# Performance work log

Hardware: AMD Instinct MI355X
Metric: run time of the kernel (lower is better)

## Reference

```python
import jax, jax.numpy as jnp
import numpy as np
from jax import lax

PLENS = [2, 3, 4, 5, 6, 7]
NPAT = 50  # patterns per length
V, WD, T, H, C = 100000, 300, 2048, 100, 2
D = sum(p * 2 * NPAT for p in PLENS)  # 2700 diag rows actually used


def setup_inputs() -> dict:
    key = jax.random.key(0)
    ks = jax.random.split(key, 20)
    inp = {}
    inp['doc'] = jax.random.randint(ks[0], (T,), 0, V)
    inp['embeddings'] = jax.random.normal(ks[1], (V, WD), jnp.float32)
    diags = jax.random.normal(ks[2], (D, WD), jnp.float32)
    diags = diags / jnp.linalg.norm(diags, axis=1, keepdims=True)  # normalize() in __init__
    inp['diags'] = diags
    inp['bias'] = jax.random.normal(ks[3], (D,), jnp.float32)
    for i, p in enumerate(PLENS):
        inp[f'eps{p}'] = jax.random.normal(ks[4 + i], (NPAT, p - 1), jnp.float32)
    inp['epsilon_scale'] = 0.5 * jnp.ones((1,), jnp.float32)
    inp['self_loop_scale'] = 0.5 * jnp.ones((1,), jnp.float32)
    tot = NPAT * len(PLENS)  # 300
    inp['w1'] = jax.random.normal(ks[10], (tot, H), jnp.float32) * 0.05
    inp['b1'] = jax.random.normal(ks[11], (H,), jnp.float32) * 0.05
    inp['w2'] = jax.random.normal(ks[12], (H, C), jnp.float32) * 0.05
    inp['b2'] = jax.random.normal(ks[13], (C,), jnp.float32) * 0.05
    return inp


def _run_group(tm, eps, sls, plen):
    # tm: [T, NPAT, 2, plen]; eps: [NPAT, plen-1]; sls: [1] (self-loop scale)
    # sum-times semiring: zero=0, one=1, plus=add, times=mul
    one_col = jnp.ones((NPAT, 1), tm.dtype)
    zero_col = jnp.zeros((NPAT, 1), tm.dtype)
    h0 = jnp.concatenate([one_col, jnp.zeros((NPAT, plen - 1), tm.dtype)], axis=1)

    def step(carry, tm_t):
        h, sc = carry
        # epsilon transitions
        h = h + jnp.concatenate([zero_col, h[:, :-1] * eps], axis=1)
        # main (word) transitions with restart padding (semiring one)
        res = jnp.concatenate([one_col, h[:, :-1] * tm_t[:, 1, :-1]], axis=1)
        # scaled self-loops
        res = res + sls * (h * tm_t[:, 0, :])
        return (res, sc + res[:, -1]), None

    (_, sc), _ = lax.scan(step, (h0, jnp.zeros((NPAT,), tm.dtype)), tm)
    return sc  # [NPAT]


def reference(doc, embeddings, diags, bias, eps2, eps3, eps4, eps5, eps6, eps7,
              epsilon_scale, self_loop_scale, w1, b1, w2, b2):
    # all per-token transition values at once: [T, D]
    tm_full = jax.nn.sigmoid(embeddings[doc] @ diags.T + bias)
    sls = jax.nn.sigmoid(self_loop_scale)
    eps_sc = jax.nn.sigmoid(epsilon_scale)
    eps_list = [eps2, eps3, eps4, eps5, eps6, eps7]
    scores = []
    start = 0
    for p, eps_raw in zip(PLENS, eps_list):
        end = start + p * 2 * NPAT
        tm = tm_full[:, start:end].reshape(-1, NPAT, 2, p)
        eps = eps_sc * jax.nn.sigmoid(eps_raw)
        scores.append(_run_group(tm, eps, sls, p))
        start = end
    s = jnp.concatenate(scores)[None, :]  # [1, total_num_patterns]
    h = jax.nn.relu(s @ w1 + b1)
    return h @ w2 + b2  # logits [1, num_classes]
```

## Files before the change

kernel.cpp:

```cpp
#include <hip/hip_runtime.h>
#include <math.h>

#define T_LEN 2048
#define WD 300
#define DTOT 2700
#define NPAT 50
#define H_DIM 100
#define NCLS 2
#define CCH 64
#define SCH 32
#define TOTPAT 300
#define RSTRIDE 68
#define KP 320
#define ASTR 40

typedef short bf16x8 __attribute__((ext_vector_type(8)));
typedef float f32x4 __attribute__((ext_vector_type(4)));

__device__ __forceinline__ float sigm(float x) { return 1.f / (1.f + __expf(-x)); }

__device__ __forceinline__ unsigned short f2bf(float x) {
    unsigned int u = __float_as_uint(x);
    u += 0x7fffu + ((u >> 16) & 1u);
    return (unsigned short)(u >> 16);
}
__device__ __forceinline__ float bf2f(unsigned short h) {
    return __uint_as_float(((unsigned int)h) << 16);
}

#define NA2 (T_LEN * (KP / 2))
#define NB2 (DTOT * (KP / 2))

__global__ __launch_bounds__(256) void prepack(const int* __restrict__ doc,
                                               const float* __restrict__ emb,
                                               const float* __restrict__ diags,
                                               unsigned short* __restrict__ Ah,
                                               unsigned short* __restrict__ Al,
                                               unsigned short* __restrict__ Bh,
                                               unsigned short* __restrict__ Bl) {
    int gid = blockIdx.x * 256 + threadIdx.x;
    float2 v = make_float2(0.f, 0.f);
    unsigned short* ph;
    unsigned short* pl;
    size_t off;
    if (gid < NA2) {
        int t = gid / (KP / 2);
        int kk = (gid - t * (KP / 2)) * 2;
        if (kk < WD) v = *(const float2*)(emb + (size_t)doc[t] * WD + kk);
        off = (size_t)t * KP + kk;
        ph = Ah; pl = Al;
    } else {
        int b = gid - NA2;
        if (b >= NB2) return;
        int n = b / (KP / 2);
        int kk = (b - n * (KP / 2)) * 2;
        if (kk < WD) v = *(const float2*)(diags + (size_t)n * WD + kk);
        off = (size_t)n * KP + kk;
        ph = Bh; pl = Bl;
    }
    unsigned short h0 = f2bf(v.x), h1 = f2bf(v.y);
    unsigned short l0 = f2bf(v.x - bf2f(h0)), l1 = f2bf(v.y - bf2f(h1));
    ushort2 hv; hv.x = h0; hv.y = h1;
    ushort2 lv; lv.x = l0; lv.y = l1;
    *(ushort2*)(ph + off) = hv;
    *(ushort2*)(pl + off) = lv;
}

__global__ __launch_bounds__(256) void gemm_mfma(const unsigned short* __restrict__ Ah,
                                                 const unsigned short* __restrict__ Al,
                                                 const unsigned short* __restrict__ Bh,
                                                 const unsigned short* __restrict__ Bl,
                                                 const float* __restrict__ bias,
                                                 float* __restrict__ Cm) {
    __shared__ unsigned short sA[2][128][ASTR];
    __shared__ unsigned short sB[2][64][ASTR];
    int tid = threadIdx.x;
    int lane = tid & 63, wid = tid >> 6;
    int m0 = blockIdx.y * 128, n0 = blockIdx.x * 64;
    int wm = (wid >> 1) * 64;
    int wn = (wid & 1) * 32;

    int srow = tid >> 2, sq = tid & 3;
    int nr = n0 + srow; if (nr > DTOT - 1) nr = DTOT - 1;
    const size_t a0off = (size_t)(m0 + srow) * KP + sq * 8;
    const size_t a1off = (size_t)(m0 + srow + 64) * KP + sq * 8;
    const size_t boff = (size_t)nr * KP + sq * 8;

    f32x4 acc[4][2];
#pragma unroll
    for (int mi = 0; mi < 4; ++mi)
#pragma unroll
        for (int ni = 0; ni < 2; ++ni) acc[mi][ni] = (f32x4)(0.f);

    uint4 pah0 = *(const uint4*)(Ah + a0off);
    uint4 pah1 = *(const uint4*)(Ah + a1off);
    uint4 pal0 = *(const uint4*)(Al + a0off);
    uint4 pal1 = *(const uint4*)(Al + a1off);
    uint4 pbh = *(const uint4*)(Bh + boff);
    uint4 pbl = *(const uint4*)(Bl + boff);

    for (int k0 = 0; k0 < KP; k0 += 32) {
        __syncthreads();
        *(uint4*)&sA[0][srow][sq * 8] = pah0;
        *(uint4*)&sA[0][srow + 64][sq * 8] = pah1;
        *(uint4*)&sA[1][srow][sq * 8] = pal0;
        *(uint4*)&sA[1][srow + 64][sq * 8] = pal1;
        *(uint4*)&sB[0][srow][sq * 8] = pbh;
        *(uint4*)&sB[1][srow][sq * 8] = pbl;
        __syncthreads();

        if (k0 + 32 < KP) {
            int kn = k0 + 32;
            pah0 = *(const uint4*)(Ah + a0off + kn);
            pah1 = *(const uint4*)(Ah + a1off + kn);
            pal0 = *(const uint4*)(Al + a0off + kn);
            pal1 = *(const uint4*)(Al + a1off + kn);
            pbh = *(const uint4*)(Bh + boff + kn);
            pbl = *(const uint4*)(Bl + boff + kn);
        }

        int kc = (lane >> 4) * 8;
        int mr = lane & 15;
        bf16x8 ah[4], al[4], bh[2], bl[2];
#pragma unroll
        for (int mi = 0; mi < 4; ++mi) {
            ah[mi] = *(bf16x8*)&sA[0][wm + mi * 16 + mr][kc];
            al[mi] = *(bf16x8*)&sA[1][wm + mi * 16 + mr][kc];
        }
#pragma unroll
        for (int ni = 0; ni < 2; ++ni) {
            bh[ni] = *(bf16x8*)&sB[0][wn + ni * 16 + mr][kc];
            bl[ni] = *(bf16x8*)&sB[1][wn + ni * 16 + mr][kc];
        }
#pragma unroll
        for (int mi = 0; mi < 4; ++mi)
#pragma unroll
            for (int ni = 0; ni < 2; ++ni) {
                acc[mi][ni] = __builtin_amdgcn_mfma_f32_16x16x32_bf16(ah[mi], bh[ni], acc[mi][ni], 0, 0, 0);
                acc[mi][ni] = __builtin_amdgcn_mfma_f32_16x16x32_bf16(ah[mi], bl[ni], acc[mi][ni], 0, 0, 0);
                acc[mi][ni] = __builtin_amdgcn_mfma_f32_16x16x32_bf16(al[mi], bh[ni], acc[mi][ni], 0, 0, 0);
            }
    }

    int mr = lane & 15;
    int rq = lane >> 4;
#pragma unroll
    for (int ni = 0; ni < 2; ++ni) {
        int col = n0 + wn + ni * 16 + mr;
        int cc = col < DTOT ? col : DTOT - 1;
        float bs = bias[cc];
        if (col < DTOT) {
#pragma unroll
            for (int mi = 0; mi < 4; ++mi)
#pragma unroll
                for (int r = 0; r < 4; ++r) {
                    int row = m0 + wm + mi * 16 + rq * 4 + r;
                    Cm[(size_t)row * DTOT + col] = sigm(acc[mi][ni][r] + bs);
                }
        }
    }
}

template <int P, int PBP>
__device__ void pass1_blk(int chunk, int patblk, const float* __restrict__ tm,
                          const float* __restrict__ epsr, float sls, float esc,
                          float* __restrict__ ws2, int g, float* __restrict__ sT,
                          int tid) {
    constexpr int NP1 = P + 1;
    constexpr int dstart = 100 * ((P * (P - 1)) / 2 - 1);
    constexpr int ROWF = PBP * 2 * P;
    constexpr int RB4 = ROWF / 4;
    constexpr int NF4 = SCH * RB4;

    const float* gbase = tm + (size_t)(chunk * SCH) * DTOT + dstart + patblk * ROWF;
#pragma unroll
    for (int i = 0; i < (NF4 + 63) / 64; ++i) {
        int f = i * 64 + tid;
        if (f < NF4) {
            int t = f / RB4;
            int q = f - t * RB4;
            *(float4*)&sT[t * ROWF + q * 4] = *(const float4*)(gbase + (size_t)t * DTOT + q * 4);
        }
    }
    __syncthreads();

    int patl = tid / NP1;
    int col = tid - patl * NP1;
    int pat = patblk * PBP + patl;
    if (patl < PBP && pat < NPAT) {
        float eps[P - 1];
#pragma unroll
        for (int j = 0; j < P - 1; ++j) eps[j] = esc * sigm(epsr[pat * (P - 1) + j]);

        float x[P];
#pragma unroll
        for (int i = 0; i < P; ++i) x[i] = 0.f;
        float inj = 0.f;
        if (col < P) x[col] = 1.f; else inj = 1.f;
        float qacc = 0.f;

        const float* lb = sT + patl * 2 * P;
#pragma unroll 4
        for (int t = 0; t < SCH; ++t) {
            float tv[2 * P];
            const float* row = lb + t * ROWF;
#pragma unroll
            for (int j = 0; j < P; ++j) {
                float2 u = *(const float2*)(row + 2 * j);
                tv[2 * j] = u.x;
                tv[2 * j + 1] = u.y;
            }
            float heps[P];
            heps[0] = x[0];
#pragma unroll
            for (int i = 1; i < P; ++i) heps[i] = fmaf(x[i - 1], eps[i - 1], x[i]);
            float res[P];
            res[0] = fmaf(heps[0], sls * tv[0], inj);
#pragma unroll
            for (int i = 1; i < P; ++i)
                res[i] = fmaf(heps[i - 1], tv[P + i - 1], heps[i] * (sls * tv[i]));
#pragma unroll
            for (int i = 0; i < P; ++i) x[i] = res[i];
            qacc += x[P - 1];
        }

        int gidx = g * NPAT + pat;
        float* dst = ws2 + ((size_t)(gidx * CCH + chunk)) * 64 + col * 8;
#pragma unroll
        for (int i = 0; i < P; ++i) dst[i] = x[i];
        dst[7] = qacc;
    }
}

__global__ __launch_bounds__(64) void pass1_kernel(const float* __restrict__ tm,
                                                   const float* __restrict__ e2,
                                                   const float* __restrict__ e3,
                                                   const float* __restrict__ e4,
                                                   const float* __restrict__ e5,
                                                   const float* __restrict__ e6,
                                                   const float* __restrict__ e7,
                                                   const float* __restrict__ eps_scale,
                                                   const float* __restrict__ sl_scale,
                                                   float* __restrict__ ws2) {
    __shared__ float sT[3584];
    int b = blockIdx.x;
    int chunk = b / 30;
    int r = b - chunk * 30;
    int tid = threadIdx.x;
    float sls = sigm(sl_scale[0]);
    float esc = sigm(eps_scale[0]);
    if (r < 3)       pass1_blk<2, 21>(chunk, r,      tm, e2, sls, esc, ws2, 0, sT, tid);
    else if (r < 7)  pass1_blk<3, 16>(chunk, r - 3,  tm, e3, sls, esc, ws2, 1, sT, tid);
    else if (r < 12) pass1_blk<4, 12>(chunk, r - 7,  tm, e4, sls, esc, ws2, 2, sT, tid);
    else if (r < 17) pass1_blk<5, 10>(chunk, r - 12, tm, e5, sls, esc, ws2, 3, sT, tid);
    else if (r < 23) pass1_blk<6, 9>(chunk, r - 17,  tm, e6, sls, esc, ws2, 4, sT, tid);
    else             pass1_blk<7, 8>(chunk, r - 23,  tm, e7, sls, esc, ws2, 5, sT, tid);
}

template <int P>
__device__ void fold_pattern(const float* __restrict__ ws2, float* __restrict__ R,
                             float* __restrict__ scores, int gidx, int tid) {
    constexpr int NP1 = P + 1;
    const float4* src = (const float4*)(ws2 + (size_t)gidx * CCH * 64);
#pragma unroll
    for (int j = 0; j < 4; ++j) {
        int f = j * 256 + tid;
        int rec = f >> 4;
        int q4 = f & 15;
        *(float4*)&R[rec * RSTRIDE + q4 * 4] = src[f];
    }
    int pair = tid / NP1;
    int col = tid - pair * NP1;
    for (int g = 1; g < CCH; g <<= 1) {
        __syncthreads();
        int npairs = CCH / (2 * g);
        if (pair < npairs) {
            float* Ar = &R[(pair * 2 * g) * RSTRIDE];
            const float* Br = &R[(pair * 2 * g + g) * RSTRIDE];
            if (col < P) {
                float MAj[P], mc[P];
#pragma unroll
                for (int i = 0; i < P; ++i) { MAj[i] = Ar[col * 8 + i]; mc[i] = 0.f; }
                float qc = Ar[col * 8 + 7];
#pragma unroll
                for (int k = 0; k < P; ++k) {
                    float a = MAj[k];
#pragma unroll
                    for (int i = 0; i < P; ++i) mc[i] = fmaf(Br[k * 8 + i], a, mc[i]);
                    qc = fmaf(Br[k * 8 + 7], a, qc);
                }
#pragma unroll
                for (int i = 0; i < P; ++i) Ar[col * 8 + i] = mc[i];
                Ar[col * 8 + 7] = qc;
            } else {
                float vA[P], vc[P];
#pragma unroll
                for (int i = 0; i < P; ++i) { vA[i] = Ar[P * 8 + i]; vc[i] = Br[P * 8 + i]; }
                float rc = Ar[P * 8 + 7] + Br[P * 8 + 7];
#pragma unroll
                for (int k = 0; k < P; ++k) {
                    float a = vA[k];
#pragma unroll
                    for (int i = 0; i < P; ++i) vc[i] = fmaf(Br[k * 8 + i], a, vc[i]);
                    rc = fmaf(Br[k * 8 + 7], a, rc);
                }
#pragma unroll
                for (int i = 0; i < P; ++i) Ar[P * 8 + i] = vc[i];
                Ar[P * 8 + 7] = rc;
            }
        }
    }
    __syncthreads();
    if (tid == 0) scores[gidx] = R[0 * 8 + 7] + R[P * 8 + 7];
}

__global__ __launch_bounds__(256) void pass2a_kernel(const float* __restrict__ ws2,
                                                     float* __restrict__ scores) {
    __shared__ float R[CCH * RSTRIDE];
    int gidx = blockIdx.x;
    int g = gidx / NPAT;
    int tid = threadIdx.x;
    switch (g) {
        case 0: fold_pattern<2>(ws2, R, scores, gidx, tid); break;
        case 1: fold_pattern<3>(ws2, R, scores, gidx, tid); break;
        case 2: fold_pattern<4>(ws2, R, scores, gidx, tid); break;
        case 3: fold_pattern<5>(ws2, R, scores, gidx, tid); break;
        case 4: fold_pattern<6>(ws2, R, scores, gidx, tid); break;
        case 5: fold_pattern<7>(ws2, R, scores, gidx, tid); break;
    }
}

__global__ __launch_bounds__(256) void mlp_kernel(const float* __restrict__ scores,
                                                  const float* __restrict__ w1,
                                                  const float* __restrict__ b1,
                                                  const float* __restrict__ w2,
                                                  const float* __restrict__ b2,
                                                  float* __restrict__ out) {
    __shared__ float w1_lds[TOTPAT * H_DIM];
    __shared__ float s_lds[TOTPAT];
    __shared__ float h_lds[H_DIM];
    int tid = threadIdx.x;
    for (int f = tid; f < (TOTPAT * H_DIM) / 4; f += 256)
        *(float4*)&w1_lds[f * 4] = *(const float4*)(w1 + f * 4);
    for (int i = tid; i < TOTPAT; i += 256) s_lds[i] = scores[i];
    __syncthreads();
    if (tid < H_DIM) {
        float a = b1[tid];
#pragma unroll 6
        for (int i = 0; i < TOTPAT; ++i) a = fmaf(s_lds[i], w1_lds[i * H_DIM + tid], a);
        h_lds[tid] = fmaxf(a, 0.f);
    }
    __syncthreads();
    if (tid < NCLS) {
        float a = b2[tid];
        for (int j = 0; j < H_DIM; ++j) a = fmaf(h_lds[j], w2[j * NCLS + tid], a);
        out[tid] = a;
    }
}

extern "C" void kernel_launch(void* const* d_in, const int* in_sizes, int n_in,
                              void* d_out, int out_size, void* d_ws, size_t ws_size,
                              hipStream_t stream) {
    const int* doc = (const int*)d_in[0];
    const float* emb = (const float*)d_in[1];
    const float* diags = (const float*)d_in[2];
    const float* bias = (const float*)d_in[3];
    const float* e2 = (const float*)d_in[4];
    const float* e3 = (const float*)d_in[5];
    const float* e4 = (const float*)d_in[6];
    const float* e5 = (const float*)d_in[7];
    const float* e6 = (const float*)d_in[8];
    const float* e7 = (const float*)d_in[9];
    const float* eps_scale = (const float*)d_in[10];
    const float* sl_scale = (const float*)d_in[11];
    const float* w1 = (const float*)d_in[12];
    const float* b1 = (const float*)d_in[13];
    const float* w2 = (const float*)d_in[14];
    const float* b2 = (const float*)d_in[15];
    float* out = (float*)d_out;

    char* ws = (char*)d_ws;
    float* tm = (float*)ws;
    float* ws2 = (float*)(ws + 22118400);
    unsigned short* Ah = (unsigned short*)(ws + 22118400);
    unsigned short* Al = (unsigned short*)(ws + 23429120);
    unsigned short* Bh = (unsigned short*)(ws + 24739840);
    unsigned short* Bl = (unsigned short*)(ws + 26467840);
    float* scores = (float*)(ws + 28195840);

    hipLaunchKernelGGL(prepack, dim3((NA2 + NB2 + 255) / 256), dim3(256), 0, stream,
                       doc, emb, diags, Ah, Al, Bh, Bl);
    hipLaunchKernelGGL(gemm_mfma, dim3((DTOT + 63) / 64, T_LEN / 128), dim3(256), 0,
                       stream, Ah, Al, Bh, Bl, bias, tm);
    hipLaunchKernelGGL(pass1_kernel, dim3(CCH * 30), dim3(64), 0, stream,
                       tm, e2, e3, e4, e5, e6, e7, eps_scale, sl_scale, ws2);
    hipLaunchKernelGGL(pass2a_kernel, dim3(TOTPAT), dim3(256), 0, stream,
                       ws2, scores);
    hipLaunchKernelGGL(mlp_kernel, dim3(1), dim3(256), 0, stream,
                       scores, w1, b1, w2, b2, out);
}
```

Baseline: 238.3 us.

## Widen GEMM N-tile to 128 and fuse MLP into last pass2 block

The GEMM block tile grows from 128x64 to 128x128 so each block reuses A across more columns, with 4x4 accumulators per wave. The separate MLP kernel is folded into the pass2 kernel: each block bumps an atomic counter (reset in prepack), and the last block runs the MLP. This removes one launch and halves the A-tile reloads, at the cost of fewer GEMM blocks, more registers, and a large static LDS allocation in every pass2 block.

```diff
diff --git a/kernel.cpp b/kernel.cpp
--- a/kernel.cpp
+++ b/kernel.cpp
@@ -37,7 +37,9 @@
                                                unsigned short* __restrict__ Ah,
                                                unsigned short* __restrict__ Al,
                                                unsigned short* __restrict__ Bh,
-                                               unsigned short* __restrict__ Bl) {
+                                               unsigned short* __restrict__ Bl,
+                                               int* __restrict__ counter) {
+    if (blockIdx.x == 0 && threadIdx.x == 0) *counter = 0;
     int gid = blockIdx.x * 256 + threadIdx.x;
     float2 v = make_float2(0.f, 0.f);
     unsigned short* ph;
@@ -73,31 +75,35 @@
                                                  const float* __restrict__ bias,
                                                  float* __restrict__ Cm) {
     __shared__ unsigned short sA[2][128][ASTR];
-    __shared__ unsigned short sB[2][64][ASTR];
+    __shared__ unsigned short sB[2][128][ASTR];
     int tid = threadIdx.x;
     int lane = tid & 63, wid = tid >> 6;
-    int m0 = blockIdx.y * 128, n0 = blockIdx.x * 64;
+    int m0 = blockIdx.y * 128, n0 = blockIdx.x * 128;
     int wm = (wid >> 1) * 64;
-    int wn = (wid & 1) * 32;
+    int wn = (wid & 1) * 64;
 
     int srow = tid >> 2, sq = tid & 3;
-    int nr = n0 + srow; if (nr > DTOT - 1) nr = DTOT - 1;
+    int nr0 = n0 + srow;       if (nr0 > DTOT - 1) nr0 = DTOT - 1;
+    int nr1 = n0 + srow + 64;  if (nr1 > DTOT - 1) nr1 = DTOT - 1;
     const size_t a0off = (size_t)(m0 + srow) * KP + sq * 8;
     const size_t a1off = (size_t)(m0 + srow + 64) * KP + sq * 8;
-    const size_t boff = (size_t)nr * KP + sq * 8;
-
-    f32x4 acc[4][2];
+    const size_t b0off = (size_t)nr0 * KP + sq * 8;
+    const size_t b1off = (size_t)nr1 * KP + sq * 8;
+
+    f32x4 acc[4][4];
 #pragma unroll
     for (int mi = 0; mi < 4; ++mi)
 #pragma unroll
-        for (int ni = 0; ni < 2; ++ni) acc[mi][ni] = (f32x4)(0.f);
+        for (int ni = 0; ni < 4; ++ni) acc[mi][ni] = (f32x4)(0.f);
 
     uint4 pah0 = *(const uint4*)(Ah + a0off);
     uint4 pah1 = *(const uint4*)(Ah + a1off);
     uint4 pal0 = *(const uint4*)(Al + a0off);
     uint4 pal1 = *(const uint4*)(Al + a1off);
-    uint4 pbh = *(const uint4*)(Bh + boff);
-    uint4 pbl = *(const uint4*)(Bl + boff);
+    uint4 pbh0 = *(const uint4*)(Bh + b0off);
+    uint4 pbh1 = *(const uint4*)(Bh + b1off);
+    uint4 pbl0 = *(const uint4*)(Bl + b0off);
+    uint4 pbl1 = *(const uint4*)(Bl + b1off);
 
     for (int k0 = 0; k0 < KP; k0 += 32) {
         __syncthreads();
@@ -105,8 +111,10 @@
         *(uint4*)&sA[0][srow + 64][sq * 8] = pah1;
         *(uint4*)&sA[1][srow][sq * 8] = pal0;
         *(uint4*)&sA[1][srow + 64][sq * 8] = pal1;
-        *(uint4*)&sB[0][srow][sq * 8] = pbh;
-        *(uint4*)&sB[1][srow][sq * 8] = pbl;
+        *(uint4*)&sB[0][srow][sq * 8] = pbh0;
+        *(uint4*)&sB[0][srow + 64][sq * 8] = pbh1;
+        *(uint4*)&sB[1][srow][sq * 8] = pbl0;
+        *(uint4*)&sB[1][srow + 64][sq * 8] = pbl1;
         __syncthreads();
 
         if (k0 + 32 < KP) {
@@ -115,27 +123,29 @@
             pah1 = *(const uint4*)(Ah + a1off + kn);
             pal0 = *(const uint4*)(Al + a0off + kn);
             pal1 = *(const uint4*)(Al + a1off + kn);
-            pbh = *(const uint4*)(Bh + boff + kn);
-            pbl = *(const uint4*)(Bl + boff + kn);
+            pbh0 = *(const uint4*)(Bh + b0off + kn);
+            pbh1 = *(const uint4*)(Bh + b1off + kn);
+            pbl0 = *(const uint4*)(Bl + b0off + kn);
+            pbl1 = *(const uint4*)(Bl + b1off + kn);
         }
 
         int kc = (lane >> 4) * 8;
         int mr = lane & 15;
-        bf16x8 ah[4], al[4], bh[2], bl[2];
+        bf16x8 ah[4], al[4], bh[4], bl[4];
 #pragma unroll
         for (int mi = 0; mi < 4; ++mi) {
             ah[mi] = *(bf16x8*)&sA[0][wm + mi * 16 + mr][kc];
             al[mi] = *(bf16x8*)&sA[1][wm + mi * 16 + mr][kc];
         }
 #pragma unroll
-        for (int ni = 0; ni < 2; ++ni) {
+        for (int ni = 0; ni < 4; ++ni) {
             bh[ni] = *(bf16x8*)&sB[0][wn + ni * 16 + mr][kc];
             bl[ni] = *(bf16x8*)&sB[1][wn + ni * 16 + mr][kc];
         }
 #pragma unroll
         for (int mi = 0; mi < 4; ++mi)
 #pragma unroll
-            for (int ni = 0; ni < 2; ++ni) {
+            for (int ni = 0; ni < 4; ++ni) {
                 acc[mi][ni] = __builtin_amdgcn_mfma_f32_16x16x32_bf16(ah[mi], bh[ni], acc[mi][ni], 0, 0, 0);
                 acc[mi][ni] = __builtin_amdgcn_mfma_f32_16x16x32_bf16(ah[mi], bl[ni], acc[mi][ni], 0, 0, 0);
                 acc[mi][ni] = __builtin_amdgcn_mfma_f32_16x16x32_bf16(al[mi], bh[ni], acc[mi][ni], 0, 0, 0);
@@ -145,11 +155,10 @@
     int mr = lane & 15;
     int rq = lane >> 4;
 #pragma unroll
-    for (int ni = 0; ni < 2; ++ni) {
+    for (int ni = 0; ni < 4; ++ni) {
         int col = n0 + wn + ni * 16 + mr;
-        int cc = col < DTOT ? col : DTOT - 1;
-        float bs = bias[cc];
         if (col < DTOT) {
+            float bs = bias[col];
 #pragma unroll
             for (int mi = 0; mi < 4; ++mi)
 #pragma unroll
@@ -314,47 +323,50 @@
     if (tid == 0) scores[gidx] = R[0 * 8 + 7] + R[P * 8 + 7];
 }
 
-__global__ __launch_bounds__(256) void pass2a_kernel(const float* __restrict__ ws2,
-                                                     float* __restrict__ scores) {
-    __shared__ float R[CCH * RSTRIDE];
+__global__ __launch_bounds__(256) void pass2_kernel(const float* __restrict__ ws2,
+                                                    float* __restrict__ scores,
+                                                    const float* __restrict__ w1,
+                                                    const float* __restrict__ b1,
+                                                    const float* __restrict__ w2,
+                                                    const float* __restrict__ b2,
+                                                    float* __restrict__ out,
+                                                    int* __restrict__ counter) {
+    __shared__ float big[TOTPAT * H_DIM];
+    __shared__ float s_lds[TOTPAT];
+    __shared__ float h_lds[H_DIM];
+    __shared__ int flag;
     int gidx = blockIdx.x;
     int g = gidx / NPAT;
     int tid = threadIdx.x;
     switch (g) {
-        case 0: fold_pattern<2>(ws2, R, scores, gidx, tid); break;
-        case 1: fold_pattern<3>(ws2, R, scores, gidx, tid); break;
-        case 2: fold_pattern<4>(ws2, R, scores, gidx, tid); break;
-        case 3: fold_pattern<5>(ws2, R, scores, gidx, tid); break;
-        case 4: fold_pattern<6>(ws2, R, scores, gidx, tid); break;
-        case 5: fold_pattern<7>(ws2, R, scores, gidx, tid); break;
-    }
-}
-
-__global__ __launch_bounds__(256) void mlp_kernel(const float* __restrict__ scores,
-                                                  const float* __restrict__ w1,
-                                                  const float* __restrict__ b1,
-                                                  const float* __restrict__ w2,
-                                                  const float* __restrict__ b2,
-                                                  float* __restrict__ out) {
-    __shared__ float w1_lds[TOTPAT * H_DIM];
-    __shared__ float s_lds[TOTPAT];
-    __shared__ float h_lds[H_DIM];
-    int tid = threadIdx.x;
-    for (int f = tid; f < (TOTPAT * H_DIM) / 4; f += 256)
-        *(float4*)&w1_lds[f * 4] = *(const float4*)(w1 + f * 4);
-    for (int i = tid; i < TOTPAT; i += 256) s_lds[i] = scores[i];
+        case 0: fold_pattern<2>(ws2, big, scores, gidx, tid); break;
+        case 1: fold_pattern<3>(ws2, big, scores, gidx, tid); break;
+        case 2: fold_pattern<4>(ws2, big, scores, gidx, tid); break;
+        case 3: fold_pattern<5>(ws2, big, scores, gidx, tid); break;
+        case 4: fold_pattern<6>(ws2, big, scores, gidx, tid); break;
+        case 5: fold_pattern<7>(ws2, big, scores, gidx, tid); break;
+    }
+    __threadfence();
+    if (tid == 0) flag = atomicAdd(counter, 1);
     __syncthreads();
-    if (tid < H_DIM) {
-        float a = b1[tid];
+    if (flag == TOTPAT - 1) {
+        __threadfence();
+        for (int f = tid; f < (TOTPAT * H_DIM) / 4; f += 256)
+            *(float4*)&big[f * 4] = *(const float4*)(w1 + f * 4);
+        for (int i = tid; i < TOTPAT; i += 256) s_lds[i] = scores[i];
+        __syncthreads();
+        if (tid < H_DIM) {
+            float a = b1[tid];
 #pragma unroll 6
-        for (int i = 0; i < TOTPAT; ++i) a = fmaf(s_lds[i], w1_lds[i * H_DIM + tid], a);
-        h_lds[tid] = fmaxf(a, 0.f);
-    }
-    __syncthreads();
-    if (tid < NCLS) {
-        float a = b2[tid];
-        for (int j = 0; j < H_DIM; ++j) a = fmaf(h_lds[j], w2[j * NCLS + tid], a);
-        out[tid] = a;
+            for (int i = 0; i < TOTPAT; ++i) a = fmaf(s_lds[i], big[i * H_DIM + tid], a);
+            h_lds[tid] = fmaxf(a, 0.f);
+        }
+        __syncthreads();
+        if (tid < NCLS) {
+            float a = b2[tid];
+            for (int j = 0; j < H_DIM; ++j) a = fmaf(h_lds[j], w2[j * NCLS + tid], a);
+            out[tid] = a;
+        }
     }
 }
 
@@ -387,15 +399,14 @@
     unsigned short* Bh = (unsigned short*)(ws + 24739840);
     unsigned short* Bl = (unsigned short*)(ws + 26467840);
     float* scores = (float*)(ws + 28195840);
+    int* counter = (int*)(ws + 28197040);
 
     hipLaunchKernelGGL(prepack, dim3((NA2 + NB2 + 255) / 256), dim3(256), 0, stream,
-                       doc, emb, diags, Ah, Al, Bh, Bl);
-    hipLaunchKernelGGL(gemm_mfma, dim3((DTOT + 63) / 64, T_LEN / 128), dim3(256), 0,
+                       doc, emb, diags, Ah, Al, Bh, Bl, counter);
+    hipLaunchKernelGGL(gemm_mfma, dim3((DTOT + 127) / 128, T_LEN / 128), dim3(256), 0,
                        stream, Ah, Al, Bh, Bl, bias, tm);
     hipLaunchKernelGGL(pass1_kernel, dim3(CCH * 30), dim3(64), 0, stream,
                        tm, e2, e3, e4, e5, e6, e7, eps_scale, sl_scale, ws2);
-    hipLaunchKernelGGL(pass2a_kernel, dim3(TOTPAT), dim3(256), 0, stream,
-                       ws2, scores);
-    hipLaunchKernelGGL(mlp_kernel, dim3(1), dim3(256), 0, stream,
-                       scores, w1, b1, w2, b2, out);
-}
+    hipLaunchKernelGGL(pass2_kernel, dim3(TOTPAT), dim3(256), 0, stream,
+                       ws2, scores, w1, b1, w2, b2, out, counter);
+}
```

Measured after the change: 254.9 us. 6.9% more time.
